# Performance work log

Hardware: AMD Instinct MI355X
Metric: run time of the kernel (lower is better)

Reference implementation:

```python
import jax, jax.numpy as jnp
import numpy as np

N_ACT = 300000
C = 128
K = 9
BATCH, H, W = 4, 1024, 1024
EPS = 1e-4  # scn BatchNormalization default eps


def _build_rulebook(rng):
    # sample N_ACT unique active sites on a (BATCH, H, W) grid
    flat = np.sort(rng.choice(BATCH * H * W, size=N_ACT, replace=False).astype(np.int64))
    b = flat // (H * W)
    y = (flat // W) % H
    x = flat % W
    nbr = np.full((N_ACT, K), -1, dtype=np.int32)
    k = 0
    for dy in (-1, 0, 1):
        for dx in (-1, 0, 1):
            ny, nx = y + dy, x + dx
            valid = (ny >= 0) & (ny < H) & (nx >= 0) & (nx < W)
            nflat = b * (H * W) + ny * W + nx
            pos = np.searchsorted(flat, nflat)
            pos_c = np.clip(pos, 0, N_ACT - 1)
            found = valid & (flat[pos_c] == nflat)
            nbr[:, k] = np.where(found, pos_c, -1).astype(np.int32)
            k += 1
    return jnp.asarray(nbr)


def setup_inputs() -> dict:
    key = jax.random.key(0)
    k1, k2, k3 = jax.random.split(key, 3)
    rng = np.random.default_rng(0)
    nbr_idx = _build_rulebook(rng)
    scale = 1.0 / np.sqrt(K * C)
    return {
        "x": jax.random.normal(k1, (N_ACT, C), dtype=jnp.float32),
        "nbr_idx": nbr_idx,
        "W1": jax.random.normal(k2, (K, C, C), dtype=jnp.float32) * scale,
        "gamma1": jnp.ones((C,), jnp.float32),
        "beta1": jnp.zeros((C,), jnp.float32),
        "W2": jax.random.normal(k3, (K, C, C), dtype=jnp.float32) * scale,
        "gamma2": jnp.ones((C,), jnp.float32),
        "beta2": jnp.zeros((C,), jnp.float32),
    }


def _subm_conv(feats, nbr_idx, Wk):
    # gather -> GEMM -> accumulate, one pass per kernel offset (K=9 fixed)
    out = jnp.zeros((feats.shape[0], Wk.shape[2]), feats.dtype)
    for k in range(Wk.shape[0]):
        idx = nbr_idx[:, k]
        mask = (idx >= 0)[:, None]
        g = jnp.where(mask, feats[jnp.maximum(idx, 0)], 0.0)
        out = out + g @ Wk[k]
    return out


def _batchnorm(feats, gamma, beta):
    mean = feats.mean(axis=0)
    var = feats.var(axis=0)  # biased, as in torch BN normalization
    return (feats - mean) * jax.lax.rsqrt(var + EPS) * gamma + beta


def reference(x, nbr_idx, W1, gamma1, beta1, W2, gamma2, beta2):
    out = _subm_conv(x, nbr_idx, W1)
    out = jax.nn.relu(_batchnorm(out, gamma1, beta1))  # BatchNormReLU
    out = _subm_conv(out, nbr_idx, W2)
    out = _batchnorm(out, gamma2, beta2)  # BatchNormalization
    return jax.nn.relu(out + x)  # AddTable + ReLU
```

## Files before the change

kernel.cpp:

```cpp
#include <hip/hip_runtime.h>


#define N_ACT 300000
#define NTAP  9
#define EPSV  1e-4f
#define GSB   2048
#define NWU   4800000

using f16x8 = __attribute__((ext_vector_type(8))) _Float16;
using f32x4 = __attribute__((ext_vector_type(4))) float;

#define OFF_PH    0UL
#define OFF_TMP   76800000UL
#define OFF_W1    230400000UL
#define OFF_W2    (OFF_W1 + 294912UL)
#define OFF_STATS (OFF_W2 + 294912UL)
#define OFF_ZBUF  (OFF_STATS + 2048UL)

__device__ __forceinline__ unsigned short f2h(float v) {
  _Float16 h = (_Float16)v;
  return __builtin_bit_cast(unsigned short, h);
}

__global__ void tohalf_prep_kernel(const float* __restrict__ x, unsigned short* __restrict__ ph,
                                   const float* __restrict__ W1, const float* __restrict__ W2,
                                   unsigned short* __restrict__ w1, unsigned short* __restrict__ w2,
                                   float* __restrict__ zstats) {
  int pb = blockIdx.x - GSB;
  if (pb >= 0) {
    int t = threadIdx.x;
    if (pb == 36) {
      for (int i = t; i < 576; i += 256) zstats[i] = 0.f;
      return;
    }
    int w = pb / 18, rem = pb % 18;
    int tap = rem >> 1, ch = rem & 1;
    const float* W = w ? W2 : W1;
    unsigned short* o = w ? w2 : w1;
    int n  = t >> 1;
    int s0 = (t & 1) * 4;
    for (int s = s0; s < s0 + 4; ++s) {
      int sigma = s ^ (n & 7);
      for (int j = 0; j < 8; ++j) {
        int   k = ch * 64 + sigma * 8 + j;
        float v = W[tap * 16384 + k * 128 + n];
        o[rem * 8192 + n * 64 + s * 8 + j] = f2h(v);
      }
    }
    return;
  }
  for (long u = blockIdx.x * 256 + threadIdx.x; u < NWU; u += (long)GSB * 256) {
    long i = u * 8;
    float4 a = *(const float4*)(x + i);
    float4 b = *(const float4*)(x + i + 4);
    uint4 p;
    p.x = (unsigned)f2h(a.x) | ((unsigned)f2h(a.y) << 16);
    p.y = (unsigned)f2h(a.z) | ((unsigned)f2h(a.w) << 16);
    p.z = (unsigned)f2h(b.x) | ((unsigned)f2h(b.y) << 16);
    p.w = (unsigned)f2h(b.z) | ((unsigned)f2h(b.w) << 16);
    *(uint4*)(ph + i) = p;
  }
}

__global__ __launch_bounds__(256, 2)
void conv_kernel(const unsigned short* __restrict__ pH, const int* __restrict__ nbr,
                 const unsigned short* __restrict__ wH,
                 unsigned short* __restrict__ outp, float* __restrict__ ssum, float* __restrict__ ssq,
                 const unsigned short* __restrict__ zbuf) {
  __shared__ char smem[65536];
  const int t  = threadIdx.x;
  const int wv = t >> 6, ln = t & 63;
  const int m0 = blockIdx.x * 128;
  const int rs = ln >> 3, sg = ln & 7;
  const int lane16 = ln & 15, g = ln >> 4;

  int idx[NTAP][4];
#pragma unroll
  for (int tap = 0; tap < NTAP; ++tap)
#pragma unroll
    for (int it = 0; it < 4; ++it) {
      int gm = m0 + wv * 32 + it * 8 + rs;
      idx[tap][it] = (gm < N_ACT) ? nbr[gm * 9 + tap] : -1;
    }

  f32x4 acc[16];
#pragma unroll
  for (int i = 0; i < 16; ++i) acc[i] = f32x4{0.f, 0.f, 0.f, 0.f};

  auto stage = [&](int c, int p) {
    const int tap = c >> 1, ch = c & 1;
#pragma unroll
    for (int it = 0; it < 4; ++it) {
      int r     = wv * 32 + it * 8 + rs;
      int sigma = sg ^ (r & 7);
      int id    = idx[tap][it];
      long off  = (long)(id >= 0 ? id : 0) * 128 + ch * 64 + sigma * 8;
      const unsigned short* gs = (id >= 0) ? (pH + off) : (zbuf + sigma * 8);
      int lo = p * 16384 + r * 128 + sg * 16;
      __builtin_amdgcn_global_load_lds((const __attribute__((address_space(1))) void*)gs,
                                       (__attribute__((address_space(3))) void*)(smem + lo), 16, 0, 0);
    }
    const char* gb = (const char*)wH + (tap * 2 + ch) * 16384;
#pragma unroll
    for (int it = 0; it < 4; ++it) {
      int o = wv * 4096 + it * 1024 + ln * 16;
      __builtin_amdgcn_global_load_lds((const __attribute__((address_space(1))) void*)(gb + o),
                                       (__attribute__((address_space(3))) void*)(smem + 32768 + p * 16384 + o), 16, 0, 0);
    }
  };

  auto compute = [&](int p) {
    const char* bufA = smem + p * 16384;
    const char* bufB = smem + 32768 + p * 16384;
#pragma unroll
    for (int ks = 0; ks < 2; ++ks) {
      f16x8 ah[4], bh[4];
      int sigma = ks * 4 + g;
#pragma unroll
      for (int mt = 0; mt < 4; ++mt) {
        int m = (wv & 1) * 64 + mt * 16 + lane16;
        ah[mt] = *(const f16x8*)(bufA + m * 128 + ((sigma ^ (m & 7)) * 16));
      }
#pragma unroll
      for (int nt = 0; nt < 4; ++nt) {
        int n = (wv >> 1) * 64 + nt * 16 + lane16;
        bh[nt] = *(const f16x8*)(bufB + n * 128 + ((sigma ^ (n & 7)) * 16));
      }
#pragma unroll
      for (int mt = 0; mt < 4; ++mt)
#pragma unroll
        for (int nt = 0; nt < 4; ++nt)
          acc[mt * 4 + nt] = __builtin_amdgcn_mfma_f32_16x16x32_f16(ah[mt], bh[nt], acc[mt * 4 + nt], 0, 0, 0);
    }
  };

  stage(0, 0);
  asm volatile("s_waitcnt vmcnt(0)" ::: "memory");
  __builtin_amdgcn_sched_barrier(0);
  __builtin_amdgcn_s_barrier();

#pragma unroll
  for (int c = 0; c < 17; ++c) {
    stage(c + 1, (c + 1) & 1);
    compute(c & 1);
    asm volatile("s_waitcnt vmcnt(0)" ::: "memory");
    __builtin_amdgcn_sched_barrier(0);
    __builtin_amdgcn_s_barrier();
  }
  compute(1);

  int rowbase = m0 + (wv & 1) * 64;
  int colbase = (wv >> 1) * 64;
  float s[4], q[4];
#pragma unroll
  for (int nt = 0; nt < 4; ++nt) { s[nt] = 0.f; q[nt] = 0.f; }
#pragma unroll
  for (int mt = 0; mt < 4; ++mt)
#pragma unroll
    for (int nt = 0; nt < 4; ++nt)
#pragma unroll
      for (int r = 0; r < 4; ++r) {
        float v  = acc[mt * 4 + nt][r];
        int  row = rowbase + mt * 16 + g * 4 + r;
        int  col = colbase + nt * 16 + lane16;
        if (row < N_ACT) outp[row * 128 + col] = f2h(v);
        s[nt] += v; q[nt] += v * v;
      }
  __syncthreads();
  float* sbuf = (float*)smem;
  float* qbuf = ((float*)smem) + 256;
#pragma unroll
  for (int nt = 0; nt < 4; ++nt) {
    float sv = s[nt], qv = q[nt];
    sv += __shfl_xor(sv, 16, 64); sv += __shfl_xor(sv, 32, 64);
    qv += __shfl_xor(qv, 16, 64); qv += __shfl_xor(qv, 32, 64);
    if (ln < 16) { sbuf[wv * 64 + nt * 16 + ln] = sv; qbuf[wv * 64 + nt * 16 + ln] = qv; }
  }
  __syncthreads();
  if (t < 128) {
    int c = t;
    float tot = (c < 64) ? (sbuf[c] + sbuf[64 + c]) : (sbuf[128 + (c - 64)] + sbuf[192 + (c - 64)]);
    atomicAdd(ssum + c, tot);
  } else {
    int c = t - 128;
    float tot = (c < 64) ? (qbuf[c] + qbuf[64 + c]) : (qbuf[128 + (c - 64)] + qbuf[192 + (c - 64)]);
    atomicAdd(ssq + c, tot);
  }
}

__global__ void bn_relu_tohalf_kernel(const unsigned short* __restrict__ tmp,
                                      const float* __restrict__ ssum, const float* __restrict__ ssq,
                                      const float* __restrict__ gamma, const float* __restrict__ beta,
                                      unsigned short* __restrict__ ph) {
  long u0 = blockIdx.x * 256 + threadIdx.x;
  int  c  = (int)((u0 * 8) & 127);
  float sc[8], bs[8];
#pragma unroll
  for (int j = 0; j < 8; ++j) {
    float mean = ssum[c + j] * (1.f / N_ACT);
    float var  = ssq[c + j] * (1.f / N_ACT) - mean * mean;
    float k    = rsqrtf(var + EPSV) * gamma[c + j];
    sc[j] = k; bs[j] = beta[c + j] - mean * k;
  }
  for (long u = u0; u < NWU; u += (long)GSB * 256) {
    long i = u * 8;
    f16x8 v = *(const f16x8*)(tmp + i);
    float y0 = fmaxf((float)v[0] * sc[0] + bs[0], 0.f);
    float y1 = fmaxf((float)v[1] * sc[1] + bs[1], 0.f);
    float y2 = fmaxf((float)v[2] * sc[2] + bs[2], 0.f);
    float y3 = fmaxf((float)v[3] * sc[3] + bs[3], 0.f);
    float y4 = fmaxf((float)v[4] * sc[4] + bs[4], 0.f);
    float y5 = fmaxf((float)v[5] * sc[5] + bs[5], 0.f);
    float y6 = fmaxf((float)v[6] * sc[6] + bs[6], 0.f);
    float y7 = fmaxf((float)v[7] * sc[7] + bs[7], 0.f);
    uint4 p;
    p.x = (unsigned)f2h(y0) | ((unsigned)f2h(y1) << 16);
    p.y = (unsigned)f2h(y2) | ((unsigned)f2h(y3) << 16);
    p.z = (unsigned)f2h(y4) | ((unsigned)f2h(y5) << 16);
    p.w = (unsigned)f2h(y6) | ((unsigned)f2h(y7) << 16);
    *(uint4*)(ph + i) = p;
  }
}

__global__ void final_kernel(const unsigned short* __restrict__ tmp,
                             const float* __restrict__ ssum, const float* __restrict__ ssq,
                             const float* __restrict__ gamma, const float* __restrict__ beta,
                             const float* __restrict__ x, float* __restrict__ outp) {
  long u0 = blockIdx.x * 256 + threadIdx.x;
  int  c  = (int)((u0 * 8) & 127);
  float sc[8], bs[8];
#pragma unroll
  for (int j = 0; j < 8; ++j) {
    float mean = ssum[c + j] * (1.f / N_ACT);
    float var  = ssq[c + j] * (1.f / N_ACT) - mean * mean;
    float k    = rsqrtf(var + EPSV) * gamma[c + j];
    sc[j] = k; bs[j] = beta[c + j] - mean * k;
  }
  for (long u = u0; u < NWU; u += (long)GSB * 256) {
    long i = u * 8;
    f16x8 v = *(const f16x8*)(tmp + i);
    float4 x0 = *(const float4*)(x + i);
    float4 x1 = *(const float4*)(x + i + 4);
    float4 o0, o1;
    o0.x = fmaxf((float)v[0] * sc[0] + bs[0] + x0.x, 0.f);
    o0.y = fmaxf((float)v[1] * sc[1] + bs[1] + x0.y, 0.f);
    o0.z = fmaxf((float)v[2] * sc[2] + bs[2] + x0.z, 0.f);
    o0.w = fmaxf((float)v[3] * sc[3] + bs[3] + x0.w, 0.f);
    o1.x = fmaxf((float)v[4] * sc[4] + bs[4] + x1.x, 0.f);
    o1.y = fmaxf((float)v[5] * sc[5] + bs[5] + x1.y, 0.f);
    o1.z = fmaxf((float)v[6] * sc[6] + bs[6] + x1.z, 0.f);
    o1.w = fmaxf((float)v[7] * sc[7] + bs[7] + x1.w, 0.f);
    *(float4*)(outp + i) = o0;
    *(float4*)(outp + i + 4) = o1;
  }
}

extern "C" void kernel_launch(void* const* d_in, const int* in_sizes, int n_in,
                              void* d_out, int out_size, void* d_ws, size_t ws_size,
                              hipStream_t stream) {
  const float* x   = (const float*)d_in[0];
  const int*   nbr = (const int*)d_in[1];
  const float* W1  = (const float*)d_in[2];
  const float* g1  = (const float*)d_in[3];
  const float* b1  = (const float*)d_in[4];
  const float* W2  = (const float*)d_in[5];
  const float* g2  = (const float*)d_in[6];
  const float* b2  = (const float*)d_in[7];
  float* out = (float*)d_out;
  char*  ws  = (char*)d_ws;

  unsigned short* ph  = (unsigned short*)(ws + OFF_PH);
  unsigned short* tmp = (unsigned short*)(ws + OFF_TMP);
  unsigned short* w1  = (unsigned short*)(ws + OFF_W1);
  unsigned short* w2  = (unsigned short*)(ws + OFF_W2);
  float*          st  = (float*)(ws + OFF_STATS);
  unsigned short* zb  = (unsigned short*)(ws + OFF_ZBUF);

  tohalf_prep_kernel<<<GSB + 37, 256, 0, stream>>>(x, ph, W1, W2, w1, w2, st);
  conv_kernel<<<2344, 256, 0, stream>>>(ph, nbr, w1, tmp, st, st + 128, zb);
  bn_relu_tohalf_kernel<<<GSB, 256, 0, stream>>>(tmp, st, st + 128, g1, b1, ph);
  conv_kernel<<<2344, 256, 0, stream>>>(ph, nbr, w2, tmp, st + 256, st + 384, zb);
  final_kernel<<<GSB, 256, 0, stream>>>(tmp, st + 256, st + 384, g2, b2, x, out);
}
```

Measured before the change: 563.1 us.

## Fuse BN1+ReLU into second sparse conv's gather stage

Removes the standalone BN-ReLU-to-half pass and instead applies BN1 scale/shift and ReLU on the fly as gathered neighbor rows are written to shared memory in a new conv_bn_kernel. This saves one full read and write of the activation tensor and a kernel launch. In exchange, each active row is normalized up to nine times (once per tap) inside the conv, adding ALU work and register pressure in the gather path. Buffers are swapped so the second conv writes into ph and final_kernel reads from it.

```diff
diff --git a/kernel.cpp b/kernel.cpp
--- a/kernel.cpp
+++ b/kernel.cpp
@@ -188,38 +188,196 @@
   }
 }
 
-__global__ void bn_relu_tohalf_kernel(const unsigned short* __restrict__ tmp,
-                                      const float* __restrict__ ssum, const float* __restrict__ ssq,
-                                      const float* __restrict__ gamma, const float* __restrict__ beta,
-                                      unsigned short* __restrict__ ph) {
-  long u0 = blockIdx.x * 256 + threadIdx.x;
-  int  c  = (int)((u0 * 8) & 127);
-  float sc[8], bs[8];
-#pragma unroll
-  for (int j = 0; j < 8; ++j) {
-    float mean = ssum[c + j] * (1.f / N_ACT);
-    float var  = ssq[c + j] * (1.f / N_ACT) - mean * mean;
-    float k    = rsqrtf(var + EPSV) * gamma[c + j];
-    sc[j] = k; bs[j] = beta[c + j] - mean * k;
-  }
-  for (long u = u0; u < NWU; u += (long)GSB * 256) {
-    long i = u * 8;
-    f16x8 v = *(const f16x8*)(tmp + i);
-    float y0 = fmaxf((float)v[0] * sc[0] + bs[0], 0.f);
-    float y1 = fmaxf((float)v[1] * sc[1] + bs[1], 0.f);
-    float y2 = fmaxf((float)v[2] * sc[2] + bs[2], 0.f);
-    float y3 = fmaxf((float)v[3] * sc[3] + bs[3], 0.f);
-    float y4 = fmaxf((float)v[4] * sc[4] + bs[4], 0.f);
-    float y5 = fmaxf((float)v[5] * sc[5] + bs[5], 0.f);
-    float y6 = fmaxf((float)v[6] * sc[6] + bs[6], 0.f);
-    float y7 = fmaxf((float)v[7] * sc[7] + bs[7], 0.f);
-    uint4 p;
-    p.x = (unsigned)f2h(y0) | ((unsigned)f2h(y1) << 16);
-    p.y = (unsigned)f2h(y2) | ((unsigned)f2h(y3) << 16);
-    p.z = (unsigned)f2h(y4) | ((unsigned)f2h(y5) << 16);
-    p.w = (unsigned)f2h(y6) | ((unsigned)f2h(y7) << 16);
-    *(uint4*)(ph + i) = p;
-  }
+__global__ __launch_bounds__(256, 2)
+void conv_bn_kernel(const unsigned short* __restrict__ pT, const int* __restrict__ nbr,
+                    const unsigned short* __restrict__ wH,
+                    const float* __restrict__ s1sum, const float* __restrict__ s1sq,
+                    const float* __restrict__ g1, const float* __restrict__ b1,
+                    unsigned short* __restrict__ outp,
+                    float* __restrict__ ssum, float* __restrict__ ssq) {
+  __shared__ char smem[65536];
+  const int t  = threadIdx.x;
+  const int wv = t >> 6, ln = t & 63;
+  const int m0 = blockIdx.x * 128;
+  const int rs = ln >> 3, sg = ln & 7;
+  const int lane16 = ln & 15, g = ln >> 4;
+  const int sig8 = (sg ^ rs) * 8;
+
+  int idx[NTAP][4];
+#pragma unroll
+  for (int tap = 0; tap < NTAP; ++tap)
+#pragma unroll
+    for (int it = 0; it < 4; ++it) {
+      int gm = m0 + wv * 32 + it * 8 + rs;
+      idx[tap][it] = (gm < N_ACT) ? nbr[gm * 9 + tap] : -1;
+    }
+
+  f32x4 scE0, scE1, bsE0, bsE1, scO0, scO1, bsO0, bsO1;
+  {
+    auto mk = [&](int base, f32x4& sc0, f32x4& sc1, f32x4& bs0, f32x4& bs1) {
+      float4 s0 = *(const float4*)(s1sum + base), s1v = *(const float4*)(s1sum + base + 4);
+      float4 q0 = *(const float4*)(s1sq  + base), q1v = *(const float4*)(s1sq  + base + 4);
+      float4 g0 = *(const float4*)(g1 + base),    g1v = *(const float4*)(g1 + base + 4);
+      float4 e0 = *(const float4*)(b1 + base),    e1v = *(const float4*)(b1 + base + 4);
+#pragma unroll
+      for (int j = 0; j < 4; ++j) {
+        float m = ((const float*)&s0)[j] * (1.f / N_ACT);
+        float v = ((const float*)&q0)[j] * (1.f / N_ACT) - m * m;
+        float k = rsqrtf(v + EPSV) * ((const float*)&g0)[j];
+        sc0[j] = k; bs0[j] = ((const float*)&e0)[j] - m * k;
+        m = ((const float*)&s1v)[j] * (1.f / N_ACT);
+        v = ((const float*)&q1v)[j] * (1.f / N_ACT) - m * m;
+        k = rsqrtf(v + EPSV) * ((const float*)&g1v)[j];
+        sc1[j] = k; bs1[j] = ((const float*)&e1v)[j] - m * k;
+      }
+    };
+    mk(sig8, scE0, scE1, bsE0, bsE1);
+    mk(64 + sig8, scO0, scO1, bsO0, bsO1);
+  }
+
+  f32x4 acc[16];
+#pragma unroll
+  for (int i = 0; i < 16; ++i) acc[i] = f32x4{0.f, 0.f, 0.f, 0.f};
+
+  auto stageB = [&](int c, int p) {
+    const char* gb = (const char*)wH + c * 16384;
+#pragma unroll
+    for (int it = 0; it < 4; ++it) {
+      int o = wv * 4096 + it * 1024 + ln * 16;
+      __builtin_amdgcn_global_load_lds((const __attribute__((address_space(1))) void*)(gb + o),
+                                       (__attribute__((address_space(3))) void*)(smem + 32768 + p * 16384 + o), 16, 0, 0);
+    }
+  };
+
+  auto compute = [&](int p) {
+    const char* bufA = smem + p * 16384;
+    const char* bufB = smem + 32768 + p * 16384;
+#pragma unroll
+    for (int ks = 0; ks < 2; ++ks) {
+      f16x8 ah[4], bh[4];
+      int sigma = ks * 4 + g;
+#pragma unroll
+      for (int mt = 0; mt < 4; ++mt) {
+        int m = (wv & 1) * 64 + mt * 16 + lane16;
+        ah[mt] = *(const f16x8*)(bufA + m * 128 + ((sigma ^ (m & 7)) * 16));
+      }
+#pragma unroll
+      for (int nt = 0; nt < 4; ++nt) {
+        int n = (wv >> 1) * 64 + nt * 16 + lane16;
+        bh[nt] = *(const f16x8*)(bufB + n * 128 + ((sigma ^ (n & 7)) * 16));
+      }
+#pragma unroll
+      for (int mt = 0; mt < 4; ++mt)
+#pragma unroll
+        for (int nt = 0; nt < 4; ++nt)
+          acc[mt * 4 + nt] = __builtin_amdgcn_mfma_f32_16x16x32_f16(ah[mt], bh[nt], acc[mt * 4 + nt], 0, 0, 0);
+    }
+  };
+
+  auto cvh = [&](unsigned hb, float sc_, float bs_) -> unsigned {
+    float f = (float)__builtin_bit_cast(_Float16, (unsigned short)(hb & 0xffff));
+    return (unsigned)f2h(fmaxf(f * sc_ + bs_, 0.f));
+  };
+  auto bnpk = [&](uint4 u, const f32x4& s0, const f32x4& s1, const f32x4& b0, const f32x4& b1v) -> uint4 {
+    uint4 o;
+    o.x = cvh(u.x, s0[0], b0[0]) | (cvh(u.x >> 16, s0[1], b0[1]) << 16);
+    o.y = cvh(u.y, s0[2], b0[2]) | (cvh(u.y >> 16, s0[3], b0[3]) << 16);
+    o.z = cvh(u.z, s1[0], b1v[0]) | (cvh(u.z >> 16, s1[1], b1v[1]) << 16);
+    o.w = cvh(u.w, s1[2], b1v[2]) | (cvh(u.w >> 16, s1[3], b1v[3]) << 16);
+    return o;
+  };
+
+  uint4 u0, u1, u2, u3;
+  int   j0, j1, j2, j3;
+
+#define ALOAD(cc)                                                              \
+  { const int tap_ = (cc) >> 1, ch_ = (cc) & 1;                                \
+    j0 = idx[tap_][0]; j1 = idx[tap_][1]; j2 = idx[tap_][2]; j3 = idx[tap_][3];\
+    const unsigned short* bp = pT + ch_ * 64 + sig8;                           \
+    u0 = *(const uint4*)(bp + (long)(j0 < 0 ? 0 : j0) * 128);                  \
+    u1 = *(const uint4*)(bp + (long)(j1 < 0 ? 0 : j1) * 128);                  \
+    u2 = *(const uint4*)(bp + (long)(j2 < 0 ? 0 : j2) * 128);                  \
+    u3 = *(const uint4*)(bp + (long)(j3 < 0 ? 0 : j3) * 128); }
+
+#define AWRITE(cc, pp)                                                         \
+  { const int ch_ = (cc) & 1;                                                  \
+    const f32x4& S0 = ch_ ? scO0 : scE0; const f32x4& S1 = ch_ ? scO1 : scE1;  \
+    const f32x4& B0 = ch_ ? bsO0 : bsE0; const f32x4& B1 = ch_ ? bsO1 : bsE1;  \
+    uint4 o0 = bnpk(u0, S0, S1, B0, B1), o1 = bnpk(u1, S0, S1, B0, B1);        \
+    uint4 o2 = bnpk(u2, S0, S1, B0, B1), o3 = bnpk(u3, S0, S1, B0, B1);        \
+    if (j0 < 0) o0 = uint4{0, 0, 0, 0};                                        \
+    if (j1 < 0) o1 = uint4{0, 0, 0, 0};                                        \
+    if (j2 < 0) o2 = uint4{0, 0, 0, 0};                                        \
+    if (j3 < 0) o3 = uint4{0, 0, 0, 0};                                        \
+    char* ab = smem + (pp) * 16384 + (wv * 32 + rs) * 128 + sg * 16;           \
+    *(uint4*)(ab)        = o0;                                                 \
+    *(uint4*)(ab + 1024) = o1;                                                 \
+    *(uint4*)(ab + 2048) = o2;                                                 \
+    *(uint4*)(ab + 3072) = o3; }
+
+  ALOAD(0);
+  stageB(0, 0);
+  asm volatile("s_waitcnt vmcnt(0)" ::: "memory");
+  __builtin_amdgcn_sched_barrier(0);
+  AWRITE(0, 0);
+  asm volatile("s_waitcnt lgkmcnt(0)" ::: "memory");
+  __builtin_amdgcn_sched_barrier(0);
+  __builtin_amdgcn_s_barrier();
+
+#pragma unroll
+  for (int c = 0; c < 17; ++c) {
+    ALOAD(c + 1);
+    stageB(c + 1, (c + 1) & 1);
+    __builtin_amdgcn_sched_barrier(0);
+    compute(c & 1);
+    asm volatile("s_waitcnt vmcnt(0)" ::: "memory");
+    __builtin_amdgcn_sched_barrier(0);
+    AWRITE(c + 1, (c + 1) & 1);
+    asm volatile("s_waitcnt lgkmcnt(0)" ::: "memory");
+    __builtin_amdgcn_sched_barrier(0);
+    __builtin_amdgcn_s_barrier();
+  }
+  compute(1);
+
+  int rowbase = m0 + (wv & 1) * 64;
+  int colbase = (wv >> 1) * 64;
+  float s[4], q[4];
+#pragma unroll
+  for (int nt = 0; nt < 4; ++nt) { s[nt] = 0.f; q[nt] = 0.f; }
+#pragma unroll
+  for (int mt = 0; mt < 4; ++mt)
+#pragma unroll
+    for (int nt = 0; nt < 4; ++nt)
+#pragma unroll
+      for (int r = 0; r < 4; ++r) {
+        float v  = acc[mt * 4 + nt][r];
+        int  row = rowbase + mt * 16 + g * 4 + r;
+        int  col = colbase + nt * 16 + lane16;
+        if (row < N_ACT) outp[row * 128 + col] = f2h(v);
+        s[nt] += v; q[nt] += v * v;
+      }
+  __syncthreads();
+  float* sbuf = (float*)smem;
+  float* qbuf = ((float*)smem) + 256;
+#pragma unroll
+  for (int nt = 0; nt < 4; ++nt) {
+    float sv = s[nt], qv = q[nt];
+    sv += __shfl_xor(sv, 16, 64); sv += __shfl_xor(sv, 32, 64);
+    qv += __shfl_xor(qv, 16, 64); qv += __shfl_xor(qv, 32, 64);
+    if (ln < 16) { sbuf[wv * 64 + nt * 16 + ln] = sv; qbuf[wv * 64 + nt * 16 + ln] = qv; }
+  }
+  __syncthreads();
+  if (t < 128) {
+    int c = t;
+    float tot = (c < 64) ? (sbuf[c] + sbuf[64 + c]) : (sbuf[128 + (c - 64)] + sbuf[192 + (c - 64)]);
+    atomicAdd(ssum + c, tot);
+  } else {
+    int c = t - 128;
+    float tot = (c < 64) ? (qbuf[c] + qbuf[64 + c]) : (qbuf[128 + (c - 64)] + qbuf[192 + (c - 64)]);
+    atomicAdd(ssq + c, tot);
+  }
+#undef ALOAD
+#undef AWRITE
 }
 
 __global__ void final_kernel(const unsigned short* __restrict__ tmp,
@@ -278,7 +436,6 @@
 
   tohalf_prep_kernel<<<GSB + 37, 256, 0, stream>>>(x, ph, W1, W2, w1, w2, st);
   conv_kernel<<<2344, 256, 0, stream>>>(ph, nbr, w1, tmp, st, st + 128, zb);
-  bn_relu_tohalf_kernel<<<GSB, 256, 0, stream>>>(tmp, st, st + 128, g1, b1, ph);
-  conv_kernel<<<2344, 256, 0, stream>>>(ph, nbr, w2, tmp, st + 256, st + 384, zb);
-  final_kernel<<<GSB, 256, 0, stream>>>(tmp, st + 256, st + 384, g2, b2, x, out);
-}
+  conv_bn_kernel<<<2344, 256, 0, stream>>>(tmp, nbr, w2, st, st + 128, g1, b1, ph, st + 256, st + 384);
+  final_kernel<<<GSB, 256, 0, stream>>>(ph, st + 256, st + 384, g2, b2, x, out);
+}
```

Result: slower. 577.4 us (+2.5%).

## Load conv weights directly into registers in MFMA fragment layout, halving LDS

Applied to the files above, without the earlier changes.

The weight prep kernel now writes fp16 weights pre-arranged in the per-lane MFMA B-fragment order. The conv kernel loads these fragments straight from global memory into registers, double-buffered across even and odd chunks, so weights no longer go through LDS. This drops the LDS weight staging and its reads, and cuts shared memory from 64KB to 32KB. In exchange it costs 64 extra VGPRs for the two weight register sets, which may hurt occupancy or cause spills under launch_bounds(256,2), and the global weight loads now sit on the critical path.

```diff
diff --git a/kernel.cpp b/kernel.cpp
--- a/kernel.cpp
+++ b/kernel.cpp
@@ -37,15 +37,15 @@
     int tap = rem >> 1, ch = rem & 1;
     const float* W = w ? W2 : W1;
     unsigned short* o = w ? w2 : w1;
-    int n  = t >> 1;
-    int s0 = (t & 1) * 4;
-    for (int s = s0; s < s0 + 4; ++s) {
-      int sigma = s ^ (n & 7);
-      for (int j = 0; j < 8; ++j) {
-        int   k = ch * 64 + sigma * 8 + j;
-        float v = W[tap * 16384 + k * 128 + n];
-        o[rem * 8192 + n * 64 + s * 8 + j] = f2h(v);
-      }
+    for (int it = 0; it < 4; ++it) {
+      int tp = it * 256 + t;
+      int ln = tp & 63, nt = (tp >> 6) & 3, ks = (tp >> 8) & 1, n6 = tp >> 9;
+      int n     = n6 * 64 + nt * 16 + (ln & 15);
+      int kbase = ch * 64 + (ks * 4 + (ln >> 4)) * 8;
+      unsigned short v8[8];
+      for (int j = 0; j < 8; ++j)
+        v8[j] = f2h(W[tap * 16384 + (kbase + j) * 128 + n]);
+      *(uint4*)(o + rem * 8192 + n6 * 4096 + ks * 2048 + nt * 512 + ln * 8) = *(uint4*)v8;
     }
     return;
   }
@@ -67,7 +67,7 @@
                  const unsigned short* __restrict__ wH,
                  unsigned short* __restrict__ outp, float* __restrict__ ssum, float* __restrict__ ssq,
                  const unsigned short* __restrict__ zbuf) {
-  __shared__ char smem[65536];
+  __shared__ char smem[32768];
   const int t  = threadIdx.x;
   const int wv = t >> 6, ln = t & 63;
   const int m0 = blockIdx.x * 128;
@@ -87,7 +87,7 @@
 #pragma unroll
   for (int i = 0; i < 16; ++i) acc[i] = f32x4{0.f, 0.f, 0.f, 0.f};
 
-  auto stage = [&](int c, int p) {
+  auto stageA = [&](int c, int p) {
     const int tap = c >> 1, ch = c & 1;
 #pragma unroll
     for (int it = 0; it < 4; ++it) {
@@ -100,54 +100,89 @@
       __builtin_amdgcn_global_load_lds((const __attribute__((address_space(1))) void*)gs,
                                        (__attribute__((address_space(3))) void*)(smem + lo), 16, 0, 0);
     }
-    const char* gb = (const char*)wH + (tap * 2 + ch) * 16384;
-#pragma unroll
-    for (int it = 0; it < 4; ++it) {
-      int o = wv * 4096 + it * 1024 + ln * 16;
-      __builtin_amdgcn_global_load_lds((const __attribute__((address_space(1))) void*)(gb + o),
-                                       (__attribute__((address_space(3))) void*)(smem + 32768 + p * 16384 + o), 16, 0, 0);
-    }
   };
 
-  auto compute = [&](int p) {
+  auto compute = [&](int p, f16x8 b0, f16x8 b1, f16x8 b2, f16x8 b3,
+                            f16x8 b4, f16x8 b5, f16x8 b6, f16x8 b7) {
     const char* bufA = smem + p * 16384;
-    const char* bufB = smem + 32768 + p * 16384;
-#pragma unroll
-    for (int ks = 0; ks < 2; ++ks) {
-      f16x8 ah[4], bh[4];
-      int sigma = ks * 4 + g;
+    {
+      f16x8 ah[4];
+      int sigma = g;
 #pragma unroll
       for (int mt = 0; mt < 4; ++mt) {
         int m = (wv & 1) * 64 + mt * 16 + lane16;
         ah[mt] = *(const f16x8*)(bufA + m * 128 + ((sigma ^ (m & 7)) * 16));
       }
 #pragma unroll
-      for (int nt = 0; nt < 4; ++nt) {
-        int n = (wv >> 1) * 64 + nt * 16 + lane16;
-        bh[nt] = *(const f16x8*)(bufB + n * 128 + ((sigma ^ (n & 7)) * 16));
-      }
-#pragma unroll
-      for (int mt = 0; mt < 4; ++mt)
-#pragma unroll
-        for (int nt = 0; nt < 4; ++nt)
-          acc[mt * 4 + nt] = __builtin_amdgcn_mfma_f32_16x16x32_f16(ah[mt], bh[nt], acc[mt * 4 + nt], 0, 0, 0);
+      for (int mt = 0; mt < 4; ++mt) {
+        acc[mt * 4 + 0] = __builtin_amdgcn_mfma_f32_16x16x32_f16(ah[mt], b0, acc[mt * 4 + 0], 0, 0, 0);
+        acc[mt * 4 + 1] = __builtin_amdgcn_mfma_f32_16x16x32_f16(ah[mt], b1, acc[mt * 4 + 1], 0, 0, 0);
+        acc[mt * 4 + 2] = __builtin_amdgcn_mfma_f32_16x16x32_f16(ah[mt], b2, acc[mt * 4 + 2], 0, 0, 0);
+        acc[mt * 4 + 3] = __builtin_amdgcn_mfma_f32_16x16x32_f16(ah[mt], b3, acc[mt * 4 + 3], 0, 0, 0);
+      }
+    }
+    {
+      f16x8 ah[4];
+      int sigma = 4 + g;
+#pragma unroll
+      for (int mt = 0; mt < 4; ++mt) {
+        int m = (wv & 1) * 64 + mt * 16 + lane16;
+        ah[mt] = *(const f16x8*)(bufA + m * 128 + ((sigma ^ (m & 7)) * 16));
+      }
+#pragma unroll
+      for (int mt = 0; mt < 4; ++mt) {
+        acc[mt * 4 + 0] = __builtin_amdgcn_mfma_f32_16x16x32_f16(ah[mt], b4, acc[mt * 4 + 0], 0, 0, 0);
+        acc[mt * 4 + 1] = __builtin_amdgcn_mfma_f32_16x16x32_f16(ah[mt], b5, acc[mt * 4 + 1], 0, 0, 0);
+        acc[mt * 4 + 2] = __builtin_amdgcn_mfma_f32_16x16x32_f16(ah[mt], b6, acc[mt * 4 + 2], 0, 0, 0);
+        acc[mt * 4 + 3] = __builtin_amdgcn_mfma_f32_16x16x32_f16(ah[mt], b7, acc[mt * 4 + 3], 0, 0, 0);
+      }
     }
   };
 
-  stage(0, 0);
+  uint4 bE0, bE1, bE2, bE3, bE4, bE5, bE6, bE7;
+  uint4 bO0, bO1, bO2, bO3, bO4, bO5, bO6, bO7;
+
+#define BC(u) __builtin_bit_cast(f16x8, u)
+#define BLOADE(cc) { const uint4* wb_ = (const uint4*)(wH + (long)(cc) * 8192 + (wv >> 1) * 4096 + (long)ln * 8); \
+    bE0 = wb_[0];   bE1 = wb_[64];  bE2 = wb_[128]; bE3 = wb_[192];            \
+    bE4 = wb_[256]; bE5 = wb_[320]; bE6 = wb_[384]; bE7 = wb_[448]; }
+#define BLOADO(cc) { const uint4* wb_ = (const uint4*)(wH + (long)(cc) * 8192 + (wv >> 1) * 4096 + (long)ln * 8); \
+    bO0 = wb_[0];   bO1 = wb_[64];  bO2 = wb_[128]; bO3 = wb_[192];            \
+    bO4 = wb_[256]; bO5 = wb_[320]; bO6 = wb_[384]; bO7 = wb_[448]; }
+
+  stageA(0, 0);
+  BLOADE(0);
+  BLOADO(1);
   asm volatile("s_waitcnt vmcnt(0)" ::: "memory");
   __builtin_amdgcn_sched_barrier(0);
   __builtin_amdgcn_s_barrier();
 
 #pragma unroll
-  for (int c = 0; c < 17; ++c) {
-    stage(c + 1, (c + 1) & 1);
-    compute(c & 1);
+  for (int tt = 0; tt < 8; ++tt) {
+    const int c = 2 * tt;
+    stageA(c + 1, 1);
+    if (tt > 0) BLOADO(c + 1);
+    compute(0, BC(bE0), BC(bE1), BC(bE2), BC(bE3), BC(bE4), BC(bE5), BC(bE6), BC(bE7));
     asm volatile("s_waitcnt vmcnt(0)" ::: "memory");
     __builtin_amdgcn_sched_barrier(0);
     __builtin_amdgcn_s_barrier();
-  }
-  compute(1);
+    stageA(c + 2, 0);
+    BLOADE(c + 2);
+    compute(1, BC(bO0), BC(bO1), BC(bO2), BC(bO3), BC(bO4), BC(bO5), BC(bO6), BC(bO7));
+    asm volatile("s_waitcnt vmcnt(0)" ::: "memory");
+    __builtin_amdgcn_sched_barrier(0);
+    __builtin_amdgcn_s_barrier();
+  }
+  stageA(17, 1);
+  BLOADO(17);
+  compute(0, BC(bE0), BC(bE1), BC(bE2), BC(bE3), BC(bE4), BC(bE5), BC(bE6), BC(bE7));
+  asm volatile("s_waitcnt vmcnt(0)" ::: "memory");
+  __builtin_amdgcn_sched_barrier(0);
+  __builtin_amdgcn_s_barrier();
+  compute(1, BC(bO0), BC(bO1), BC(bO2), BC(bO3), BC(bO4), BC(bO5), BC(bO6), BC(bO7));
+#undef BLOADE
+#undef BLOADO
+#undef BC
 
   int rowbase = m0 + (wv & 1) * 64;
   int colbase = (wv >> 1) * 64;
```

Measured after the change: 620.7 us. 1.1x slower.
